# Kernel optimization log

Hardware: AMD Instinct MI355X
Metric: run time of the kernel (lower is better)

The kernel has to match this reference:

```python
import jax, jax.numpy as jnp
import numpy as np

N = 20000      # n_nodes
E = 320000     # n_edges (multiple of 4, so _from_coo drops nothing)
D = 512        # embed_dim
H = 8          # num_heads
DK = D // H    # d_k = 64


def setup_inputs() -> dict:
    key = jax.random.key(0)
    ks = jax.random.split(key, 12)
    x = jax.random.normal(ks[0], (N, D), jnp.float32)
    rows = jnp.sort(jax.random.randint(ks[1], (E,), 0, N))
    cols = jax.random.randint(ks[2], (E,), 0, N)
    edge_index = jnp.stack([rows, cols]).astype(jnp.int32)  # [2, E]
    att_bias = jax.random.normal(ks[3], (E, H), jnp.float32)
    s = float(1.0 / np.sqrt(D))  # ~xavier scale
    Wq = jax.random.normal(ks[4], (D, D), jnp.float32) * s
    Wk = jax.random.normal(ks[5], (D, D), jnp.float32) * s
    Wv = jax.random.normal(ks[6], (D, D), jnp.float32) * s
    Wo = jax.random.normal(ks[7], (D, D), jnp.float32) * s
    bq = jnp.zeros((D,), jnp.float32)
    bk = jnp.zeros((D,), jnp.float32)
    bv = jnp.zeros((D,), jnp.float32)
    bo = jnp.zeros((D,), jnp.float32)
    return dict(x=x, edge_index=edge_index, att_bias=att_bias,
                Wq=Wq, bq=bq, Wk=Wk, bk=bk, Wv=Wv, bv=bv, Wo=Wo, bo=bo)


def reference(x, edge_index, att_bias, Wq, bq, Wk, bk, Wv, bv, Wo, bo):
    n = x.shape[0]
    rows, cols = edge_index[0], edge_index[1]
    # per-head projections: [n, H, DK]
    q = (x @ Wq + bq).reshape(n, H, DK)
    k = (x @ Wk + bk).reshape(n, H, DK)
    v = (x @ Wv + bv).reshape(n, H, DK)
    scale = 1.0 / jnp.sqrt(jnp.asarray(DK, x.dtype))
    # masked QK^T on the edge pattern, plus additive bias: [E, H]
    logits = jnp.einsum('ehd,ehd->eh', q[rows] * scale, k[cols]) + att_bias
    # CSR (segment) softmax over each destination row
    row_max = jax.ops.segment_max(logits, rows, num_segments=n)      # [n, H]
    p = jnp.exp(logits - row_max[rows])                              # [E, H]
    denom = jax.ops.segment_sum(p, rows, num_segments=n)            # [n, H]
    att = p / denom[rows]                                            # [E, H]
    # sparse-dense bmm: y[i] = sum_{e: rows[e]=i} att[e] * v[cols[e]]
    y = jax.ops.segment_sum(att[:, :, None] * v[cols], rows, num_segments=n)  # [n, H, DK]
    out = y.reshape(n, H * DK) @ Wo + bo
    return out
```

## Files before the change

### kernel.cpp

```cpp
#include <hip/hip_runtime.h>
#include <hip/hip_bf16.h>

typedef unsigned short ushort_t;
typedef unsigned int uint32;
typedef __attribute__((ext_vector_type(8))) short short8;
typedef __attribute__((ext_vector_type(4))) float floatx4;

#define DEV __device__ __forceinline__

DEV float b2f(ushort_t u) { return __uint_as_float(((uint32)u) << 16); }
DEV ushort_t f2b(float f) {
  __hip_bfloat16 h = __float2bfloat16(f);
  return __builtin_bit_cast(unsigned short, h);
}
DEV void unpack8(const uint4& u, float* f) {
  f[0] = __uint_as_float(u.x << 16); f[1] = __uint_as_float(u.x & 0xffff0000u);
  f[2] = __uint_as_float(u.y << 16); f[3] = __uint_as_float(u.y & 0xffff0000u);
  f[4] = __uint_as_float(u.z << 16); f[5] = __uint_as_float(u.z & 0xffff0000u);
  f[6] = __uint_as_float(u.w << 16); f[7] = __uint_as_float(u.w & 0xffff0000u);
}
DEV void unpack_i8x8(uint2 u, float* f) {
  f[0] = (float)((int)(u.x << 24) >> 24);
  f[1] = (float)((int)(u.x << 16) >> 24);
  f[2] = (float)((int)(u.x << 8) >> 24);
  f[3] = (float)((int)u.x >> 24);
  f[4] = (float)((int)(u.y << 24) >> 24);
  f[5] = (float)((int)(u.y << 16) >> 24);
  f[6] = (float)((int)(u.y << 8) >> 24);
  f[7] = (float)((int)u.y >> 24);
}

#define GLOAD_LDS(gp, lp) \
  __builtin_amdgcn_global_load_lds((const __attribute__((address_space(1))) uint32*)(gp), \
                                   (__attribute__((address_space(3))) uint32*)(lp), 16, 0, 0)

#define KVROW 1088

__global__ __launch_bounds__(256) void k_detect(const ushort_t* __restrict__ x,
                                                int* __restrict__ flag) {
  __shared__ int red[256];
  int tid = threadIdx.x;
  int wild = 0;
  for (int i = tid; i < 4096; i += 256) {
    uint32 e = (x[i] >> 7) & 0xFFu;
    if (e < 100u || e > 140u) wild++;
  }
  red[tid] = wild;
  __syncthreads();
  for (int s = 128; s > 0; s >>= 1) {
    if (tid < s) red[tid] += red[tid + s];
    __syncthreads();
  }
  if (tid == 0) flag[0] = (red[0] > 400) ? 1 : 0;
}

__global__ __launch_bounds__(256) void k_transpose(
    const void* __restrict__ Wq, const void* __restrict__ Wk,
    const void* __restrict__ Wv, const void* __restrict__ Wo,
    ushort_t* __restrict__ WT4, const int* __restrict__ flagp) {
  __shared__ ushort_t t[32][33];
  int isf32 = *flagp;
  int z = blockIdx.z;
  const void* src = (z == 0) ? Wq : (z == 1) ? Wk : (z == 2) ? Wv : Wo;
  ushort_t* dst = WT4 + (size_t)z * 512 * 512;
  int bx = blockIdx.x, by = blockIdx.y;
  int tx = threadIdx.x, ty = threadIdx.y;
#pragma unroll
  for (int i = 0; i < 4; i++) {
    size_t idx = (size_t)(by * 32 + ty + 8 * i) * 512 + bx * 32 + tx;
    ushort_t v = isf32 ? f2b(((const float*)src)[idx]) : ((const ushort_t*)src)[idx];
    t[ty + 8 * i][tx] = v;
  }
  __syncthreads();
#pragma unroll
  for (int i = 0; i < 4; i++)
    dst[(size_t)(bx * 32 + ty + 8 * i) * 512 + by * 32 + tx] = t[tx][ty + 8 * i];
}

__global__ __launch_bounds__(256) void k_biases(
    const void* __restrict__ bq, const void* __restrict__ bk,
    const void* __restrict__ bv, const void* __restrict__ bo,
    float* __restrict__ biasf, const int* __restrict__ flagp) {
  int i = blockIdx.x * 256 + threadIdx.x;
  if (i >= 2048) return;
  int z = i >> 9, j = i & 511;
  const void* b = (z == 0) ? bq : (z == 1) ? bk : (z == 2) ? bv : bo;
  biasf[i] = (*flagp) ? ((const float*)b)[j] : b2f(((const ushort_t*)b)[j]);
}

__global__ __launch_bounds__(256) void k_convx(
    const void* __restrict__ x, ushort_t* __restrict__ xb, int n8,
    const int* __restrict__ flagp) {
  int i = blockIdx.x * 256 + threadIdx.x;
  if (i >= n8) return;
  if (*flagp) {
    const float* xf = (const float*)x + (size_t)i * 8;
    float4 f0 = ((const float4*)xf)[0];
    float4 f1 = ((const float4*)xf)[1];
    uint4 o;
    o.x = (uint32)f2b(f0.x) | ((uint32)f2b(f0.y) << 16);
    o.y = (uint32)f2b(f0.z) | ((uint32)f2b(f0.w) << 16);
    o.z = (uint32)f2b(f1.x) | ((uint32)f2b(f1.y) << 16);
    o.w = (uint32)f2b(f1.z) | ((uint32)f2b(f1.w) << 16);
    ((uint4*)xb)[i] = o;
  } else {
    ((uint4*)xb)[i] = ((const uint4*)x)[i];
  }
}

__global__ void k_build_rp(const int* __restrict__ rows, int E, int N, int* __restrict__ rp) {
  int i = blockIdx.x * blockDim.x + threadIdx.x;
  if (i > N) return;
  int lo = 0, hi = E;
  while (lo < hi) {
    int mid = (lo + hi) >> 1;
    if (rows[mid] < i) lo = mid + 1; else hi = mid;
  }
  rp[i] = lo;
}

DEV void gemm_body(const ushort_t* __restrict__ A, const ushort_t* __restrict__ BT,
                   const float* __restrict__ bias, void* C,
                   int M, int ldc, float scale, int row0, int by, int mode) {
  __shared__ ushort_t As[128 * 32];
  __shared__ ushort_t Bs[128 * 32];
  int tid = threadIdx.x;
  int w = tid >> 6, lane = tid & 63;
  int sr = lane >> 2;
  int sk = (lane & 3) * 8;

  floatx4 acc[4][4];
#pragma unroll
  for (int i = 0; i < 4; i++)
#pragma unroll
    for (int j = 0; j < 4; j++)
#pragma unroll
      for (int r = 0; r < 4; r++) acc[i][j][r] = 0.f;

  int lm = lane & 15, quad = lane >> 4;
  int wr = w >> 1, wc = w & 1;
  const int nG = by * 128 + w * 32;

  int rA0 = row0 + w * 32 + sr; if (rA0 >= M) rA0 = M - 1;
  int rA1 = rA0 + 16;          if (rA1 >= M) rA1 = M - 1;
  const ushort_t* gA0 = A + (size_t)rA0 * 512 + sk;
  const ushort_t* gA1 = A + (size_t)rA1 * 512 + sk;
  const ushort_t* gB0 = BT + (size_t)(nG + sr) * 512 + sk;
  const ushort_t* gB1 = BT + (size_t)(nG + 16 + sr) * 512 + sk;

  for (int k0 = 0; k0 < 512; k0 += 32) {
    GLOAD_LDS(gA0 + k0, As + (w * 32 + 0) * 32);
    GLOAD_LDS(gA1 + k0, As + (w * 32 + 16) * 32);
    GLOAD_LDS(gB0 + k0, Bs + (w * 32 + 0) * 32);
    GLOAD_LDS(gB1 + k0, Bs + (w * 32 + 16) * 32);
    __syncthreads();

    const ushort_t* pa = As + (wr * 64 + lm) * 32 + quad * 8;
    const ushort_t* pb = Bs + (wc * 64 + lm) * 32 + quad * 8;
    short8 af[4], bfr[4];
#pragma unroll
    for (int t4 = 0; t4 < 4; t4++) {
      af[t4]  = *(const short8*)(pa + t4 * 16 * 32);
      bfr[t4] = *(const short8*)(pb + t4 * 16 * 32);
    }
#pragma unroll
    for (int mt = 0; mt < 4; mt++)
#pragma unroll
      for (int nt = 0; nt < 4; nt++)
        acc[mt][nt] = __builtin_amdgcn_mfma_f32_16x16x32_bf16(af[mt], bfr[nt], acc[mt][nt], 0, 0, 0);
    __syncthreads();
  }

  int colB = by * 128 + wc * 64 + lm;
  float bv4[4];
#pragma unroll
  for (int nt = 0; nt < 4; nt++) bv4[nt] = bias[colB + nt * 16];

  if (mode <= 1) {
#pragma unroll
    for (int mt = 0; mt < 4; mt++) {
      int rg0 = row0 + wr * 64 + mt * 16 + quad * 4;
#pragma unroll
      for (int nt = 0; nt < 4; nt++) {
#pragma unroll
        for (int r = 0; r < 4; r++) {
          int rg = rg0 + r;
          if (rg < M) {
            float val = (acc[mt][nt][r] + bv4[nt]) * scale;
            size_t off = (size_t)rg * ldc + colB + nt * 16;
            if (mode == 1) ((float*)C)[off] = val;
            else           ((ushort_t*)C)[off] = f2b(val);
          }
        }
      }
    }
  } else {
    int vslot = (mode == 4);
    int colbase = by * 128 + wc * 64;
    int head = colbase >> 6;
#pragma unroll
    for (int mt = 0; mt < 4; mt++) {
#pragma unroll
      for (int r = 0; r < 4; r++) {
        int rg = row0 + wr * 64 + mt * 16 + quad * 4 + r;
        float v0 = acc[mt][0][r] + bv4[0];
        float v1 = acc[mt][1][r] + bv4[1];
        float v2 = acc[mt][2][r] + bv4[2];
        float v3 = acc[mt][3][r] + bv4[3];
        float am = fmaxf(fmaxf(fabsf(v0), fabsf(v1)), fmaxf(fabsf(v2), fabsf(v3)));
        am = fmaxf(am, __shfl_xor(am, 1));
        am = fmaxf(am, __shfl_xor(am, 2));
        am = fmaxf(am, __shfl_xor(am, 4));
        am = fmaxf(am, __shfl_xor(am, 8));
        am = fmaxf(am, 1e-20f);
        float inv8 = 127.0f / am;
        float sc8 = am * (1.0f / 127.0f);
        if (rg < M) {
          unsigned char* Crow = (unsigned char*)C + (size_t)rg * KVROW + colbase + (vslot ? 512 : 0);
          Crow[lm +  0] = (unsigned char)(signed char)(int)rintf(v0 * inv8);
          Crow[lm + 16] = (unsigned char)(signed char)(int)rintf(v1 * inv8);
          Crow[lm + 32] = (unsigned char)(signed char)(int)rintf(v2 * inv8);
          Crow[lm + 48] = (unsigned char)(signed char)(int)rintf(v3 * inv8);
          if (lm == 0)
            *(float*)((unsigned char*)C + (size_t)rg * KVROW + 1024 + head * 8 + vslot * 4) = sc8;
        }
      }
    }
  }
}

__global__ __launch_bounds__(256) void k_gemm_qkv(
    const ushort_t* __restrict__ xb, const ushort_t* __restrict__ WT4,
    const float* __restrict__ biasf, ushort_t* Qp, unsigned char* KV8, int M) {
  int z = blockIdx.z;
  const ushort_t* BT = WT4 + (size_t)z * 512 * 512;
  const float* bias = biasf + (size_t)z * 512;
  if (z == 0)
    gemm_body(xb, BT, bias, Qp, M, 512, 0.125f, blockIdx.x * 128, blockIdx.y, 0);
  else
    gemm_body(xb, BT, bias, KV8, M, 0, 1.0f, blockIdx.x * 128, blockIdx.y, z == 1 ? 3 : 4);
}

__global__ __launch_bounds__(256) void k_gemm_out(
    const ushort_t* __restrict__ y, const ushort_t* __restrict__ WT4,
    const float* __restrict__ biasf, void* out, int M,
    const int* __restrict__ flagp) {
  gemm_body(y, WT4 + (size_t)3 * 512 * 512, biasf + 3 * 512, out, M, 512, 1.0f,
            blockIdx.x * 128, blockIdx.y, *flagp);
}

__global__ __launch_bounds__(256) void k_edge(
    ushort_t* Qy, const unsigned char* __restrict__ KV8,
    const void* __restrict__ ab, const int* __restrict__ cols,
    const int* __restrict__ rp, int Nn, int E, const int* __restrict__ flagp) {
  int node = blockIdx.x * 4 + (threadIdx.x >> 6);
  if (node >= Nn) return;
  int lane = threadIdx.x & 63;
  int h8 = lane >> 3;
  int isf32 = *flagp;

  uint4 qu = ((const uint4*)(Qy + (size_t)node * 512))[lane];
  float qf[8];
  unpack8(qu, qf);

  int e0 = rp[node], e1 = rp[node + 1];
  int cnt = e1 - e0;

  float s0 = 0.f, s1 = 0.f;
  float acc0[8], acc1[8];
#pragma unroll
  for (int j = 0; j < 8; j++) { acc0[j] = 0.f; acc1[j] = 0.f; }

  uint2 kb[4], vb[4];
  float2 scb[4];
  float abf[4];

  auto pref = [&](int t, int slot) {
    int valid = t < cnt;
    int ei = valid ? (e0 + t) : e0;
    int c = valid ? cols[ei] : 0;
    const unsigned char* kvrow = KV8 + (size_t)c * KVROW;
    kb[slot] = *(const uint2*)(kvrow + lane * 8);
    vb[slot] = *(const uint2*)(kvrow + 512 + lane * 8);
    scb[slot] = *(const float2*)(kvrow + 1024 + h8 * 8);
    size_t bi = (size_t)ei * 8 + h8;
    float a = isf32 ? ((const float*)ab)[bi] : b2f(((const ushort_t*)ab)[bi]);
    abf[slot] = valid ? a : -1e30f;
  };
  auto consume = [&](int slot, float* acc, float& s) {
    float kf[8];
    unpack_i8x8(kb[slot], kf);
    float d = 0.f;
#pragma unroll
    for (int j = 0; j < 8; j++) d = fmaf(qf[j], kf[j], d);
    d += __shfl_xor(d, 1);
    d += __shfl_xor(d, 2);
    d += __shfl_xor(d, 4);
    float logit = fminf(fmaf(d, scb[slot].x, abf[slot]), 80.f);
    float pw = __expf(logit);
    s += pw;
    float pwv = pw * scb[slot].y;
    float vf[8];
    unpack_i8x8(vb[slot], vf);
#pragma unroll
    for (int j = 0; j < 8; j++) acc[j] = fmaf(pwv, vf[j], acc[j]);
  };

  pref(0, 0); pref(1, 1); pref(2, 2); pref(3, 3);
  int iters = (cnt + 3) >> 2;
  for (int it = 0; it < iters; ++it) {
    int nt = it * 4 + 4;
    consume(0, acc0, s0); pref(nt + 0, 0);
    consume(1, acc1, s1); pref(nt + 1, 1);
    consume(2, acc0, s0); pref(nt + 2, 2);
    consume(3, acc1, s1); pref(nt + 3, 3);
  }

  float s = s0 + s1;
  float inv = (cnt > 0 && s > 0.f) ? 1.f / s : 0.f;
  ushort_t hb[8];
#pragma unroll
  for (int j = 0; j < 8; j++) hb[j] = f2b((acc0[j] + acc1[j]) * inv);
  uint4 uh;
  uh.x = (uint32)hb[0] | ((uint32)hb[1] << 16);
  uh.y = (uint32)hb[2] | ((uint32)hb[3] << 16);
  uh.z = (uint32)hb[4] | ((uint32)hb[5] << 16);
  uh.w = (uint32)hb[6] | ((uint32)hb[7] << 16);
  ((uint4*)(Qy + (size_t)node * 512))[lane] = uh;
}

extern "C" void kernel_launch(void* const* d_in, const int* in_sizes, int n_in,
                              void* d_out, int out_size, void* d_ws, size_t ws_size,
                              hipStream_t stream) {
  const void* x  = d_in[0];
  const int* ei  = (const int*)d_in[1];
  const void* ab = d_in[2];
  const void* Wq = d_in[3];
  const void* bq = d_in[4];
  const void* Wk = d_in[5];
  const void* bk = d_in[6];
  const void* Wv = d_in[7];
  const void* bv = d_in[8];
  const void* Wo = d_in[9];
  const void* bo = d_in[10];

  const int D = 512;
  int M = in_sizes[0] / D;
  int E = in_sizes[1] / 2;
  const int* rows = ei;
  const int* cols = ei + E;

  char* p = (char*)d_ws;
  size_t off = 0;
  auto carve = [&](size_t bytes) -> void* {
    off = (off + 255) & ~(size_t)255;
    void* r = p + off;
    off += bytes;
    return r;
  };
  int* flag          = (int*)carve(4);
  ushort_t* WT4      = (ushort_t*)carve((size_t)4 * 512 * 512 * 2);
  float* biasf       = (float*)carve((size_t)4 * 512 * 4);
  ushort_t* xb       = (ushort_t*)carve((size_t)M * 512 * 2);
  ushort_t* Qp       = (ushort_t*)carve((size_t)M * 512 * 2);
  unsigned char* KV8 = (unsigned char*)carve((size_t)M * KVROW);
  int* rp            = (int*)carve((size_t)(M + 1) * 4);
  (void)ws_size;

  k_detect<<<1, 256, 0, stream>>>((const ushort_t*)x, flag);
  k_transpose<<<dim3(16, 16, 4), dim3(32, 8), 0, stream>>>(Wq, Wk, Wv, Wo, WT4, flag);
  k_biases<<<8, 256, 0, stream>>>(bq, bk, bv, bo, biasf, flag);
  int n8 = M * 512 / 8;
  k_convx<<<(n8 + 255) / 256, 256, 0, stream>>>(x, xb, n8, flag);
  k_build_rp<<<(M + 1 + 255) / 256, 256, 0, stream>>>(rows, E, M, rp);

  int rb = (M + 127) / 128;
  k_gemm_qkv<<<dim3(rb, 4, 3), 256, 0, stream>>>(xb, WT4, biasf, Qp, KV8, M);
  k_edge<<<(M + 3) / 4, 256, 0, stream>>>(Qp, KV8, ab, cols, rp, M, E, flag);
  k_gemm_out<<<dim3(rb, 4, 1), 256, 0, stream>>>(Qp, WT4, biasf, d_out, M, flag);
}
```

Measured before the change: 303.8 us.

## Interleave int8 K/V per lane, use sdot4 for QK, deepen edge prefetch to six

The QKV GEMM epilogue now writes K and V int8 bytes interleaved in 8-byte groups, so each lane in the edge kernel fetches its K and V slices with one 16-byte load instead of two 8-byte loads. When the sdot4 builtin is available, Q is quantized per head to int8 and the QK dot product uses integer dot4 instructions in place of unpacking and float FMAs. The software prefetch pipeline grows from 4 to 6 in-flight edges, which raises register use. Quantizing Q adds rounding error to the logits.

```diff
diff --git a/kernel.cpp b/kernel.cpp
--- a/kernel.cpp
+++ b/kernel.cpp
@@ -7,6 +7,15 @@
 typedef __attribute__((ext_vector_type(4))) float floatx4;
 
 #define DEV __device__ __forceinline__
+
+#if defined(__has_builtin)
+#if __has_builtin(__builtin_amdgcn_sdot4)
+#define HAS_SDOT 1
+#endif
+#endif
+#ifndef HAS_SDOT
+#define HAS_SDOT 0
+#endif
 
 DEV float b2f(ushort_t u) { return __uint_as_float(((uint32)u) << 16); }
 DEV ushort_t f2b(float f) {
@@ -216,13 +225,14 @@
         float inv8 = 127.0f / am;
         float sc8 = am * (1.0f / 127.0f);
         if (rg < M) {
-          unsigned char* Crow = (unsigned char*)C + (size_t)rg * KVROW + colbase + (vslot ? 512 : 0);
-          Crow[lm +  0] = (unsigned char)(signed char)(int)rintf(v0 * inv8);
-          Crow[lm + 16] = (unsigned char)(signed char)(int)rintf(v1 * inv8);
-          Crow[lm + 32] = (unsigned char)(signed char)(int)rintf(v2 * inv8);
-          Crow[lm + 48] = (unsigned char)(signed char)(int)rintf(v3 * inv8);
+          unsigned char* Crow = (unsigned char*)C + (size_t)rg * KVROW;
+          unsigned char* bp = Crow + 2 * colbase + 16 * (lm >> 3) + 8 * vslot + (lm & 7);
+          bp[ 0] = (unsigned char)(signed char)(int)rintf(v0 * inv8);
+          bp[32] = (unsigned char)(signed char)(int)rintf(v1 * inv8);
+          bp[64] = (unsigned char)(signed char)(int)rintf(v2 * inv8);
+          bp[96] = (unsigned char)(signed char)(int)rintf(v3 * inv8);
           if (lm == 0)
-            *(float*)((unsigned char*)C + (size_t)rg * KVROW + 1024 + head * 8 + vslot * 4) = sc8;
+            *(float*)(Crow + 1024 + head * 8 + vslot * 4) = sc8;
         }
       }
     }
@@ -263,6 +273,23 @@
   float qf[8];
   unpack8(qu, qf);
 
+#if HAS_SDOT
+  float qa = 0.f;
+#pragma unroll
+  for (int j = 0; j < 8; j++) qa = fmaxf(qa, fabsf(qf[j]));
+  qa = fmaxf(qa, __shfl_xor(qa, 1));
+  qa = fmaxf(qa, __shfl_xor(qa, 2));
+  qa = fmaxf(qa, __shfl_xor(qa, 4));
+  qa = fmaxf(qa, 1e-20f);
+  float qs = qa * (1.0f / 127.0f);
+  float qinv = 127.0f / qa;
+  int qp0 = 0, qp1 = 0;
+#pragma unroll
+  for (int j = 0; j < 4; j++) qp0 |= (((int)rintf(qf[j] * qinv)) & 0xFF) << (8 * j);
+#pragma unroll
+  for (int j = 4; j < 8; j++) qp1 |= (((int)rintf(qf[j] * qinv)) & 0xFF) << (8 * (j - 4));
+#endif
+
   int e0 = rp[node], e1 = rp[node + 1];
   int cnt = e1 - e0;
 
@@ -271,25 +298,33 @@
 #pragma unroll
   for (int j = 0; j < 8; j++) { acc0[j] = 0.f; acc1[j] = 0.f; }
 
-  uint2 kb[4], vb[4];
-  float2 scb[4];
-  float abf[4];
+  uint4 kvb[6];
+  float2 scb[6];
+  float abf[6];
 
   auto pref = [&](int t, int slot) {
     int valid = t < cnt;
     int ei = valid ? (e0 + t) : e0;
     int c = valid ? cols[ei] : 0;
     const unsigned char* kvrow = KV8 + (size_t)c * KVROW;
-    kb[slot] = *(const uint2*)(kvrow + lane * 8);
-    vb[slot] = *(const uint2*)(kvrow + 512 + lane * 8);
+    kvb[slot] = *(const uint4*)(kvrow + lane * 16);
     scb[slot] = *(const float2*)(kvrow + 1024 + h8 * 8);
     size_t bi = (size_t)ei * 8 + h8;
     float a = isf32 ? ((const float*)ab)[bi] : b2f(((const ushort_t*)ab)[bi]);
     abf[slot] = valid ? a : -1e30f;
   };
   auto consume = [&](int slot, float* acc, float& s) {
+#if HAS_SDOT
+    int di = __builtin_amdgcn_sdot4(qp0, (int)kvb[slot].x, 0, false);
+    di = __builtin_amdgcn_sdot4(qp1, (int)kvb[slot].y, di, false);
+    di += __shfl_xor(di, 1);
+    di += __shfl_xor(di, 2);
+    di += __shfl_xor(di, 4);
+    float logit = fminf(fmaf((float)di * qs, scb[slot].x, abf[slot]), 80.f);
+#else
     float kf[8];
-    unpack_i8x8(kb[slot], kf);
+    uint2 ku; ku.x = kvb[slot].x; ku.y = kvb[slot].y;
+    unpack_i8x8(ku, kf);
     float d = 0.f;
 #pragma unroll
     for (int j = 0; j < 8; j++) d = fmaf(qf[j], kf[j], d);
@@ -297,23 +332,28 @@
     d += __shfl_xor(d, 2);
     d += __shfl_xor(d, 4);
     float logit = fminf(fmaf(d, scb[slot].x, abf[slot]), 80.f);
+#endif
     float pw = __expf(logit);
     s += pw;
     float pwv = pw * scb[slot].y;
     float vf[8];
-    unpack_i8x8(vb[slot], vf);
+    uint2 vu; vu.x = kvb[slot].z; vu.y = kvb[slot].w;
+    unpack_i8x8(vu, vf);
 #pragma unroll
     for (int j = 0; j < 8; j++) acc[j] = fmaf(pwv, vf[j], acc[j]);
   };
 
-  pref(0, 0); pref(1, 1); pref(2, 2); pref(3, 3);
-  int iters = (cnt + 3) >> 2;
+  pref(0, 0); pref(1, 1); pref(2, 2);
+  pref(3, 3); pref(4, 4); pref(5, 5);
+  int iters = (cnt + 5) / 6;
   for (int it = 0; it < iters; ++it) {
-    int nt = it * 4 + 4;
+    int nt = it * 6 + 6;
     consume(0, acc0, s0); pref(nt + 0, 0);
     consume(1, acc1, s1); pref(nt + 1, 1);
     consume(2, acc0, s0); pref(nt + 2, 2);
     consume(3, acc1, s1); pref(nt + 3, 3);
+    consume(4, acc0, s0); pref(nt + 4, 4);
+    consume(5, acc1, s1); pref(nt + 5, 5);
   }
 
   float s = s0 + s1;
```

New measurement: 301.5 us. About the same (-0.8%).
